# Performance work log

Hardware: AMD Instinct MI355X
Metric: run time of the kernel (lower is better)

The kernel has to match this reference:

```python
import jax, jax.numpy as jnp
import numpy as np

NEG_SLOPE = 0.2

def setup_inputs() -> dict:
    key = jax.random.key(0)
    ks = jax.random.split(key, 6)
    N, C, H, E_DIM, E = 50000, 128, 64, 16, 800000
    x = jax.random.normal(ks[0], (N, C), dtype=jnp.float32)
    edge_index = jax.random.randint(ks[1], (2, E), 0, N, dtype=jnp.int64)
    edge_attr = jax.random.normal(ks[2], (E, E_DIM), dtype=jnp.float32)
    fc_w = jax.random.normal(ks[3], (H, C), dtype=jnp.float32) * (1.0 / np.sqrt(C))
    fc_b = jnp.zeros((H,), dtype=jnp.float32)
    att_w = jax.random.normal(ks[4], (H, 2 * H + E_DIM), dtype=jnp.float32) * (1.0 / np.sqrt(2 * H + E_DIM))
    att_b = jnp.zeros((H,), dtype=jnp.float32)
    return {"x": x, "edge_index": edge_index, "edge_attr": edge_attr,
            "fc_w": fc_w, "fc_b": fc_b, "att_w": att_w, "att_b": att_b}

def reference(x, edge_index, edge_attr, fc_w, fc_b, att_w, att_b):
    # Node projection: h = fc(x), [N, H]
    h = x @ fc_w.T + fc_b
    src = edge_index[0]  # i (destination of aggregation)
    dst = edge_index[1]  # j (neighbor whose features are aggregated)
    h_i = h[src]                      # [E, H]
    h_j = h[dst]                      # [E, H]
    feat = jnp.concatenate([h_i, h_j, edge_attr], axis=-1)  # [E, 2H+edge_dim]
    alpha = jax.nn.leaky_relu(feat @ att_w.T + att_b, negative_slope=NEG_SLOPE)  # [E, H]
    # dropout is identity in eval mode (training=False)
    msg = h_j * alpha                 # [E, H]
    out = jax.ops.segment_sum(msg, src, num_segments=h.shape[0])  # scatter-add into out[i]
    return out
```

## Files before the change

### kernel.cpp

```cpp
#include <hip/hip_runtime.h>


__device__ __forceinline__ unsigned bf16r(float f) {
    unsigned u = __float_as_uint(f);
    return (u + 0x7fffu + ((u >> 16) & 1u)) >> 16;
}
__device__ __forceinline__ float bf_lo(unsigned p) { return __uint_as_float(p << 16); }
__device__ __forceinline__ float bf_hi(unsigned p) { return __uint_as_float(p & 0xffff0000u); }

__global__ __launch_bounds__(256) void node_kernel(
    const float* __restrict__ x,
    const float* __restrict__ fc_w, const float* __restrict__ fc_b,
    const float* __restrict__ att_w, const float* __restrict__ att_b,
    float* __restrict__ ai_out, unsigned* __restrict__ hj_out, int N)
{
    __shared__ __align__(16) float4 wF[64 * 32];
    __shared__ __align__(16) float4 wI[64 * 16];
    __shared__ __align__(16) float4 wJ[64 * 16];
    __shared__ __align__(16) float xs[4][128];
    __shared__ __align__(16) float hs[4][64];

    const int t = threadIdx.x;
    for (int idx = t; idx < 64 * 32; idx += 256) {
        int l = idx >> 5, c = idx & 31;
        wF[l * 32 + (c ^ (l & 31))] =
            *reinterpret_cast<const float4*>(fc_w + l * 128 + c * 4);
    }
    for (int idx = t; idx < 64 * 16; idx += 256) {
        int l = idx >> 4, c = idx & 15;
        wI[l * 16 + (c ^ (l & 15))] =
            *reinterpret_cast<const float4*>(att_w + l * 144 + c * 4);
        wJ[l * 16 + (c ^ (l & 15))] =
            *reinterpret_cast<const float4*>(att_w + l * 144 + 64 + c * 4);
    }
    __syncthreads();

    const int w = t >> 6, l = t & 63;
    const float bF = fc_b[l];
    const float bA = att_b[l];
    const int waveId = blockIdx.x * 4 + w;
    const int nWaves = gridDim.x * 4;

    for (int n = waveId; n < N; n += nWaves) {
        float2 xv = reinterpret_cast<const float2*>(x)[(size_t)n * 64 + l];
        xs[w][2 * l] = xv.x;
        xs[w][2 * l + 1] = xv.y;
        float acc = bF;
        #pragma unroll
        for (int c = 0; c < 32; ++c) {
            float4 wv = wF[l * 32 + (c ^ (l & 31))];
            float4 xc = *reinterpret_cast<const float4*>(&xs[w][c * 4]);
            acc = fmaf(wv.x, xc.x, acc);
            acc = fmaf(wv.y, xc.y, acc);
            acc = fmaf(wv.z, xc.z, acc);
            acc = fmaf(wv.w, xc.w, acc);
        }
        hs[w][l] = acc;
        float a2 = bA, a3 = 0.f;
        #pragma unroll
        for (int c = 0; c < 16; ++c) {
            float4 hvv = *reinterpret_cast<const float4*>(&hs[w][c * 4]);
            float4 wi = wI[l * 16 + (c ^ (l & 15))];
            float4 wj = wJ[l * 16 + (c ^ (l & 15))];
            a2 = fmaf(wi.x, hvv.x, a2); a2 = fmaf(wi.y, hvv.y, a2);
            a2 = fmaf(wi.z, hvv.z, a2); a2 = fmaf(wi.w, hvv.w, a2);
            a3 = fmaf(wj.x, hvv.x, a3); a3 = fmaf(wj.y, hvv.y, a3);
            a3 = fmaf(wj.z, hvv.z, a3); a3 = fmaf(wj.w, hvv.w, a3);
        }
        ai_out[(size_t)n * 64 + l] = a2;
        hj_out[(size_t)n * 64 + l] = (bf16r(a3) << 16) | bf16r(acc);
    }
}

__global__ __launch_bounds__(256) void hist_kernel(
    const int* __restrict__ ei, int* __restrict__ count, int E)
{
    int i = blockIdx.x * 256 + threadIdx.x;
    int stride = gridDim.x * 256;
    for (; i < E; i += stride) atomicAdd(&count[ei[i]], 1);
}

__global__ __launch_bounds__(256) void scan1_kernel(
    const int* __restrict__ count, int* __restrict__ start,
    int* __restrict__ bsum, int N)
{
    __shared__ int wsum[4];
    const int t = threadIdx.x, blk = blockIdx.x;
    const int idx0 = blk * 1024 + t * 4;
    int c0 = 0, c1 = 0, c2 = 0, c3 = 0;
    if (idx0 + 3 < N) {
        int4 c = *reinterpret_cast<const int4*>(count + idx0);
        c0 = c.x; c1 = c.y; c2 = c.z; c3 = c.w;
    } else {
        if (idx0 + 0 < N) c0 = count[idx0 + 0];
        if (idx0 + 1 < N) c1 = count[idx0 + 1];
        if (idx0 + 2 < N) c2 = count[idx0 + 2];
    }
    const int s = c0 + c1 + c2 + c3;
    const int lane = t & 63, w = t >> 6;
    int v = s;
    #pragma unroll
    for (int off = 1; off < 64; off <<= 1) {
        int u = __shfl_up(v, off);
        if (lane >= off) v += u;
    }
    if (lane == 63) wsum[w] = v;
    __syncthreads();
    int base = 0;
    if (w > 0) base += wsum[0];
    if (w > 1) base += wsum[1];
    if (w > 2) base += wsum[2];
    const int excl = base + v - s;
    if (idx0 + 0 < N) start[idx0 + 0] = excl;
    if (idx0 + 1 < N) start[idx0 + 1] = excl + c0;
    if (idx0 + 2 < N) start[idx0 + 2] = excl + c0 + c1;
    if (idx0 + 3 < N) start[idx0 + 3] = excl + c0 + c1 + c2;
    if (t == 255) bsum[blk] = base + v;
}

__global__ void scan2_kernel(int* __restrict__ bsum, int nb)
{
    const int l = threadIdx.x;
    int v = (l < nb) ? bsum[l] : 0;
    int inc = v;
    #pragma unroll
    for (int off = 1; off < 64; off <<= 1) {
        int u = __shfl_up(inc, off);
        if (l >= off) inc += u;
    }
    if (l < nb) bsum[l] = inc - v;
}

__global__ __launch_bounds__(256) void scan3_kernel(
    int* __restrict__ start, const int* __restrict__ bsum, int N)
{
    const int blk = blockIdx.x;
    const int add = bsum[blk];
    #pragma unroll
    for (int q = 0; q < 4; ++q) {
        int i = blk * 1024 + q * 256 + threadIdx.x;
        if (i < N) start[i] += add;
    }
}

__global__ __launch_bounds__(256) void scatter_kernel(
    const int* __restrict__ ei, int* __restrict__ start,
    int2* __restrict__ sd, int E)
{
    int i = blockIdx.x * 256 + threadIdx.x;
    int stride = gridDim.x * 256;
    for (; i < E; i += stride) {
        int s = ei[i];
        int pos = atomicAdd(&start[s], 1);
        sd[pos] = make_int2(ei[E + i], i);
    }
}

__global__ __launch_bounds__(256) void reorder_kernel(
    const int2* __restrict__ sd, const float4* __restrict__ ea4,
    uint4* __restrict__ eaS, int E)
{
    int j = blockIdx.x * 256 + threadIdx.x;
    if (j >= E) return;
    int eid = sd[j].y;
    float4 r0 = ea4[(size_t)eid * 4 + 0], r1 = ea4[(size_t)eid * 4 + 1];
    float4 r2 = ea4[(size_t)eid * 4 + 2], r3 = ea4[(size_t)eid * 4 + 3];
    uint4 q0 = make_uint4((bf16r(r0.y) << 16) | bf16r(r0.x),
                          (bf16r(r0.w) << 16) | bf16r(r0.z),
                          (bf16r(r1.y) << 16) | bf16r(r1.x),
                          (bf16r(r1.w) << 16) | bf16r(r1.z));
    uint4 q1 = make_uint4((bf16r(r2.y) << 16) | bf16r(r2.x),
                          (bf16r(r2.w) << 16) | bf16r(r2.z),
                          (bf16r(r3.y) << 16) | bf16r(r3.x),
                          (bf16r(r3.w) << 16) | bf16r(r3.z));
    eaS[(size_t)j * 2 + 0] = q0;
    eaS[(size_t)j * 2 + 1] = q1;
}

__global__ __launch_bounds__(256) void csr_edge_kernel(
    const int2* __restrict__ sd, const uint2* __restrict__ eaS2,
    const int* __restrict__ endp, const int* __restrict__ count,
    const float* __restrict__ ai, const unsigned* __restrict__ hj,
    const float* __restrict__ att_w, float* __restrict__ out, int N)
{
    __shared__ uint2 eas[4][256];
    __shared__ float weS[64][17];

    const int t = threadIdx.x, w = t >> 6, l = t & 63;
    for (int idx = t; idx < 1024; idx += 256)
        weS[idx >> 4][idx & 15] = att_w[(idx >> 4) * 144 + 128 + (idx & 15)];
    __syncthreads();

    const int n = blockIdx.x * 4 + w;
    if (n >= N) return;

    float we[16];
    #pragma unroll
    for (int k = 0; k < 16; ++k) we[k] = weS[l][k];

    const int deg = count[n];
    const int base = endp[n] - deg;
    const float aiv = ai[(size_t)n * 64 + l];
    float acc = 0.f;

#define EDGE_BODY(KK, UU)                                                      \
    {                                                                          \
        float pre = aiv + bf_hi(UU);                                           \
        _Pragma("unroll") for (int r = 0; r < 4; ++r) {                        \
            uint2 q = eas[w][(KK) * 4 + r];                                    \
            pre = fmaf(we[r * 4 + 0], bf_lo(q.x), pre);                        \
            pre = fmaf(we[r * 4 + 1], bf_hi(q.x), pre);                        \
            pre = fmaf(we[r * 4 + 2], bf_lo(q.y), pre);                        \
            pre = fmaf(we[r * 4 + 3], bf_hi(q.y), pre);                        \
        }                                                                      \
        float alpha = pre > 0.f ? pre : 0.2f * pre;                            \
        acc = fmaf(bf_lo(UU), alpha, acc);                                     \
    }

    int done = 0;
    while (done < deg) {
        const int rem = min(64, deg - done);
        int v = 0;
        if (l < rem) v = sd[base + done + l].x;
        for (int f = l; f < rem * 4; f += 64)
            eas[w][f] = eaS2[(size_t)(base + done) * 4 + f];
        int k = 0;
        for (; k + 8 <= rem; k += 8) {
            int d[8]; unsigned u[8];
            #pragma unroll
            for (int j = 0; j < 8; ++j) {
                d[j] = __shfl(v, k + j);
                u[j] = hj[(size_t)d[j] * 64 + l];
            }
            #pragma unroll
            for (int j = 0; j < 8; ++j) EDGE_BODY(k + j, u[j]);
        }
        for (; k < rem; ++k) {
            int dd = __shfl(v, k);
            unsigned uu = hj[(size_t)dd * 64 + l];
            EDGE_BODY(k, uu);
        }
        done += rem;
    }
#undef EDGE_BODY
    out[(size_t)n * 64 + l] = acc;
}

extern "C" void kernel_launch(void* const* d_in, const int* in_sizes, int n_in,
                              void* d_out, int out_size, void* d_ws, size_t ws_size,
                              hipStream_t stream) {
    const float* x     = (const float*)d_in[0];
    const int*   ei    = (const int*)d_in[1];
    const float* ea    = (const float*)d_in[2];
    const float* fc_w  = (const float*)d_in[3];
    const float* fc_b  = (const float*)d_in[4];
    const float* att_w = (const float*)d_in[5];
    const float* att_b = (const float*)d_in[6];
    float* out = (float*)d_out;

    const int N = in_sizes[0] / 128;
    const int E = in_sizes[2] / 16;

    char* p = (char*)d_ws;
    auto align256 = [](size_t v) { return (v + 255) & ~(size_t)255; };
    float*    ai    = (float*)p;        p += align256((size_t)N * 64 * 4);
    unsigned* hj    = (unsigned*)p;     p += align256((size_t)N * 64 * 4);
    int*      count = (int*)p;          p += align256((size_t)N * 4);
    int*      startp= (int*)p;          p += align256((size_t)N * 4);
    int*      bsum  = (int*)p;          p += align256(64 * 4);
    int2*     sd    = (int2*)p;         p += align256((size_t)E * 8);
    uint4*    eaS   = (uint4*)p;

    hipMemsetAsync(count, 0, (size_t)N * sizeof(int), stream);

    node_kernel<<<512, 256, 0, stream>>>(x, fc_w, fc_b, att_w, att_b, ai, hj, N);
    hist_kernel<<<1024, 256, 0, stream>>>(ei, count, E);

    const int nb1 = (N + 1023) / 1024;
    scan1_kernel<<<nb1, 256, 0, stream>>>(count, startp, bsum, N);
    scan2_kernel<<<1, 64, 0, stream>>>(bsum, nb1);
    scan3_kernel<<<nb1, 256, 0, stream>>>(startp, bsum, N);

    scatter_kernel<<<1024, 256, 0, stream>>>(ei, startp, sd, E);
    reorder_kernel<<<(E + 255) / 256, 256, 0, stream>>>(sd, (const float4*)ea, eaS, E);

    csr_edge_kernel<<<(N + 3) / 4, 256, 0, stream>>>(
        sd, (const uint2*)eaS, startp, count, ai, hj, att_w, out, N);
}
```

Baseline: 253.6 us.

## Fuse edge-attribute reorder into CSR edge kernel, gathering fp32 attrs directly

Removes the separate reorder kernel that gathered edge_attr by edge id, packed it to bf16 and wrote a sorted copy. The CSR edge kernel now has each lane gather its edge's 16 fp32 attributes straight from the original array into padded shared memory, then runs the dot products on float4 reads. This drops one launch and a full write plus re-read of the sorted attribute buffer. In exchange the gathers are scattered 64-byte fp32 reads instead of contiguous bf16 reads. It also uses an explicit lgkmcnt wait rather than a barrier, which relies on each wave only reading its own shared-memory slice.

```diff
diff --git a/kernel.cpp b/kernel.cpp
--- a/kernel.cpp
+++ b/kernel.cpp
@@ -156,34 +156,13 @@
     }
 }
 
-__global__ __launch_bounds__(256) void reorder_kernel(
+__global__ __launch_bounds__(256) void csr_edge_kernel(
     const int2* __restrict__ sd, const float4* __restrict__ ea4,
-    uint4* __restrict__ eaS, int E)
-{
-    int j = blockIdx.x * 256 + threadIdx.x;
-    if (j >= E) return;
-    int eid = sd[j].y;
-    float4 r0 = ea4[(size_t)eid * 4 + 0], r1 = ea4[(size_t)eid * 4 + 1];
-    float4 r2 = ea4[(size_t)eid * 4 + 2], r3 = ea4[(size_t)eid * 4 + 3];
-    uint4 q0 = make_uint4((bf16r(r0.y) << 16) | bf16r(r0.x),
-                          (bf16r(r0.w) << 16) | bf16r(r0.z),
-                          (bf16r(r1.y) << 16) | bf16r(r1.x),
-                          (bf16r(r1.w) << 16) | bf16r(r1.z));
-    uint4 q1 = make_uint4((bf16r(r2.y) << 16) | bf16r(r2.x),
-                          (bf16r(r2.w) << 16) | bf16r(r2.z),
-                          (bf16r(r3.y) << 16) | bf16r(r3.x),
-                          (bf16r(r3.w) << 16) | bf16r(r3.z));
-    eaS[(size_t)j * 2 + 0] = q0;
-    eaS[(size_t)j * 2 + 1] = q1;
-}
-
-__global__ __launch_bounds__(256) void csr_edge_kernel(
-    const int2* __restrict__ sd, const uint2* __restrict__ eaS2,
     const int* __restrict__ endp, const int* __restrict__ count,
     const float* __restrict__ ai, const unsigned* __restrict__ hj,
     const float* __restrict__ att_w, float* __restrict__ out, int N)
 {
-    __shared__ uint2 eas[4][256];
+    __shared__ __align__(16) float4 eas4[4][64][5];
     __shared__ float weS[64][17];
 
     const int t = threadIdx.x, w = t >> 6, l = t & 63;
@@ -205,14 +184,19 @@
 
 #define EDGE_BODY(KK, UU)                                                      \
     {                                                                          \
+        float4 v0 = eas4[w][KK][0];                                            \
+        float4 v1 = eas4[w][KK][1];                                            \
+        float4 v2 = eas4[w][KK][2];                                            \
+        float4 v3 = eas4[w][KK][3];                                            \
         float pre = aiv + bf_hi(UU);                                           \
-        _Pragma("unroll") for (int r = 0; r < 4; ++r) {                        \
-            uint2 q = eas[w][(KK) * 4 + r];                                    \
-            pre = fmaf(we[r * 4 + 0], bf_lo(q.x), pre);                        \
-            pre = fmaf(we[r * 4 + 1], bf_hi(q.x), pre);                        \
-            pre = fmaf(we[r * 4 + 2], bf_lo(q.y), pre);                        \
-            pre = fmaf(we[r * 4 + 3], bf_hi(q.y), pre);                        \
-        }                                                                      \
+        pre = fmaf(we[0], v0.x, pre);  pre = fmaf(we[1], v0.y, pre);           \
+        pre = fmaf(we[2], v0.z, pre);  pre = fmaf(we[3], v0.w, pre);           \
+        pre = fmaf(we[4], v1.x, pre);  pre = fmaf(we[5], v1.y, pre);           \
+        pre = fmaf(we[6], v1.z, pre);  pre = fmaf(we[7], v1.w, pre);           \
+        pre = fmaf(we[8], v2.x, pre);  pre = fmaf(we[9], v2.y, pre);           \
+        pre = fmaf(we[10], v2.z, pre); pre = fmaf(we[11], v2.w, pre);          \
+        pre = fmaf(we[12], v3.x, pre); pre = fmaf(we[13], v3.y, pre);          \
+        pre = fmaf(we[14], v3.z, pre); pre = fmaf(we[15], v3.w, pre);          \
         float alpha = pre > 0.f ? pre : 0.2f * pre;                            \
         acc = fmaf(bf_lo(UU), alpha, acc);                                     \
     }
@@ -220,23 +204,32 @@
     int done = 0;
     while (done < deg) {
         const int rem = min(64, deg - done);
-        int v = 0;
-        if (l < rem) v = sd[base + done + l].x;
-        for (int f = l; f < rem * 4; f += 64)
-            eas[w][f] = eaS2[(size_t)(base + done) * 4 + f];
+        int2 v = make_int2(0, 0);
+        if (l < rem) v = sd[base + done + l];
+        {
+            const float4* er = ea4 + (size_t)v.y * 4;
+            float4 r0 = er[0], r1 = er[1], r2 = er[2], r3 = er[3];
+            eas4[w][l][0] = r0;
+            eas4[w][l][1] = r1;
+            eas4[w][l][2] = r2;
+            eas4[w][l][3] = r3;
+        }
+        asm volatile("s_waitcnt lgkmcnt(0)" ::: "memory");
+        __builtin_amdgcn_sched_barrier(0);
+
         int k = 0;
         for (; k + 8 <= rem; k += 8) {
             int d[8]; unsigned u[8];
             #pragma unroll
             for (int j = 0; j < 8; ++j) {
-                d[j] = __shfl(v, k + j);
+                d[j] = __shfl(v.x, k + j);
                 u[j] = hj[(size_t)d[j] * 64 + l];
             }
             #pragma unroll
             for (int j = 0; j < 8; ++j) EDGE_BODY(k + j, u[j]);
         }
         for (; k < rem; ++k) {
-            int dd = __shfl(v, k);
+            int dd = __shfl(v.x, k);
             unsigned uu = hj[(size_t)dd * 64 + l];
             EDGE_BODY(k, uu);
         }
@@ -268,8 +261,7 @@
     int*      count = (int*)p;          p += align256((size_t)N * 4);
     int*      startp= (int*)p;          p += align256((size_t)N * 4);
     int*      bsum  = (int*)p;          p += align256(64 * 4);
-    int2*     sd    = (int2*)p;         p += align256((size_t)E * 8);
-    uint4*    eaS   = (uint4*)p;
+    int2*     sd    = (int2*)p;
 
     hipMemsetAsync(count, 0, (size_t)N * sizeof(int), stream);
 
@@ -282,8 +274,7 @@
     scan3_kernel<<<nb1, 256, 0, stream>>>(startp, bsum, N);
 
     scatter_kernel<<<1024, 256, 0, stream>>>(ei, startp, sd, E);
-    reorder_kernel<<<(E + 255) / 256, 256, 0, stream>>>(sd, (const float4*)ea, eaS, E);
 
     csr_edge_kernel<<<(N + 3) / 4, 256, 0, stream>>>(
-        sd, (const uint2*)eaS, startp, count, ai, hj, att_w, out, N);
-}
+        sd, (const float4*)ea, startp, count, ai, hj, att_w, out, N);
+}
```

After: 248.4 us. -2.0%, faster.
